# Kernel tuning notes

Measured on AMD Instinct MI355X. Metric: run time of the kernel, lower is better.

The kernel has to match this reference:

```python
import jax, jax.numpy as jnp
import numpy as np

B = 512
D = 512          # d_in == d_out for every layer
L = 3            # number of SprecherLayerBlocks
PHI_K = 100      # knots of monotonic phi spline
PHI_CAP_K = 100  # knots of Phi spline
PHI_IN = (-10.0, 10.0)
PHI_OUT = (-10.0, 10.0)


def setup_inputs() -> dict:
    key = jax.random.key(0)
    ks = jax.random.split(key, 8)
    x = jax.random.uniform(ks[0], (B, D), dtype=jnp.float32)
    # per-layer lambda vectors ~ N(0, 2/d_in)
    lambdas = jax.random.normal(ks[1], (L, D), dtype=jnp.float32) * np.sqrt(2.0 / D)
    eta = jnp.full((L,), 1.0 / (D + 10), dtype=jnp.float32)
    # monotonic phi: log_increments = log(1/K + 1e-6), identical per layer at init
    phi_log_inc = jnp.full((L, PHI_K), np.log(1.0 / PHI_K + 1e-6), dtype=jnp.float32)
    # Phi coeffs: linspace over codomain + small noise
    base = jnp.linspace(PHI_OUT[0], PHI_OUT[1], PHI_CAP_K, dtype=jnp.float32)
    Phi_coeffs = base[None, :] + jax.random.normal(ks[2], (L, PHI_CAP_K), dtype=jnp.float32) * 0.01
    # shared trainable range params (center/radius of domain & codomain)
    dc = jnp.float32((PHI_IN[0] + PHI_IN[1]) / 2.0)
    dr = jnp.float32((PHI_IN[1] - PHI_IN[0]) / 2.0)
    cc = jnp.float32((PHI_OUT[0] + PHI_OUT[1]) / 2.0)
    cr = jnp.float32((PHI_OUT[1] - PHI_OUT[0]) / 2.0)
    res_w = jnp.full((L,), 0.1, dtype=jnp.float32)
    output_scale = jnp.float32(1.0)
    return {"x": x, "lambdas": lambdas, "eta": eta, "phi_log_inc": phi_log_inc,
            "Phi_coeffs": Phi_coeffs, "dc": dc, "dr": dr, "cc": cc, "cr": cr,
            "res_w": res_w, "output_scale": output_scale}


def _interp(x, knots, coeffs, num_knots):
    # piecewise-linear eval: searchsorted + gather + lerp (x assumed pre-clamped)
    idx = jnp.clip(jnp.searchsorted(knots, x) - 1, 0, num_knots - 2)
    k0 = knots[idx]
    t = (x - k0) / (knots[idx + 1] - k0)
    return (1.0 - t) * coeffs[idx] + t * coeffs[idx + 1]


def reference(x, lambdas, eta, phi_log_inc, Phi_coeffs, dc, dr, cc, cr, res_w, output_scale):
    eps = 1e-8
    phi_knots = jnp.linspace(0.0, 1.0, PHI_K)
    norm_knots = jnp.linspace(0.0, 1.0, PHI_CAP_K)
    in_min, in_max = dc - dr, dc + dr
    out_min, out_max = cc - cr, cc + cr
    Phi_knots = norm_knots * (in_max - in_min) + in_min
    q = jnp.arange(D, dtype=x.dtype)  # q_values, Q_VALUES_FACTOR = 1
    h = x
    for l in range(L):
        # [B, d_in, d_out] shifted inputs, clamped to phi's (0,1) domain
        shifted = jnp.clip(h[:, :, None] + eta[l] * q[None, None, :], 0.0, 1.0)
        # monotonic phi coefficients in (0,1)
        inc = jax.nn.softplus(phi_log_inc[l])
        cum = jnp.cumsum(inc)
        phi_coef = cum / (cum[-1] + eps)
        phi_out = _interp(shifted, phi_knots, phi_coef, PHI_K)
        s = jnp.einsum('bio,i->bo', phi_out, lambdas[l]) + q
        # Phi spline with trainable range + renormalization by initial coeff min/max
        sc = jnp.clip(s, in_min, in_max)
        raw = _interp(sc, Phi_knots, Phi_coeffs[l], PHI_CAP_K)
        cmin = jax.lax.stop_gradient(Phi_coeffs[l].min())
        cmax = jax.lax.stop_gradient(Phi_coeffs[l].max())
        raw_n = jnp.clip((raw - cmin) / (cmax - cmin + eps), 0.0, 1.0)
        act = out_min + (out_max - out_min) * raw_n
        act = act + res_w[l] * h  # residual (d_in == d_out)
        if l == L - 1:
            act = act.sum(axis=1, keepdims=True)  # is_final block -> [B, 1]
        h = act
    return h * output_scale
```

## Files before the change

### kernel.cpp

```cpp
#include <hip/hip_runtime.h>

#define DD 512
#define LL 3
#define KK 100

#define WS_PHI     0
#define WS_CAP     600
#define WS_INMIN   1200
#define WS_INMAX   1201
#define WS_USCALE  1202
#define WS_OUTMIN  1203
#define WS_OUTSPAN 1204
#define WS_CMIN    1205
#define WS_INVDEN  1208
#define WS_OBEGIN  1211
#define WS_OEND    1214

__device__ __forceinline__ float fract_pos(float x) {
#if __has_builtin(__builtin_amdgcn_fractf)
  return __builtin_amdgcn_fractf(x);
#else
  return x - floorf(x);
#endif
}

__device__ __forceinline__ float med3f(float x, float lo, float hi) {
#if __has_builtin(__builtin_amdgcn_fmed3f)
  return __builtin_amdgcn_fmed3f(x, lo, hi);
#else
  return fminf(fmaxf(x, lo), hi);
#endif
}

__global__ __launch_bounds__(64) void prep_kernel(
    const float* __restrict__ lambdas,
    const float* __restrict__ phi_log_inc,
    const float* __restrict__ Phi_coeffs,
    const float* __restrict__ dc, const float* __restrict__ dr,
    const float* __restrict__ cc, const float* __restrict__ cr,
    float* __restrict__ ws)
{
  const int l = blockIdx.x;
  const int t = threadIdx.x;
  __shared__ float scum[104];

  const float in_min  = dc[0] - dr[0];
  const float in_max  = dc[0] + dr[0];
  const float out_min = cc[0] - cr[0];
  const float out_max = cc[0] + cr[0];
  if (l == 0 && t == 0) {
    ws[WS_INMIN]   = in_min;
    ws[WS_INMAX]   = in_max;
    ws[WS_USCALE]  = 99.0f / (in_max - in_min);
    ws[WS_OUTMIN]  = out_min;
    ws[WS_OUTSPAN] = out_max - out_min;
  }

  float a = log1pf(expf(phi_log_inc[l*KK + t]));
  #pragma unroll
  for (int d = 1; d < 64; d <<= 1) { float n = __shfl_up(a, d, 64); if (t >= d) a += n; }
  const float totA = __shfl(a, 63, 64);
  float b = (t < 36) ? log1pf(expf(phi_log_inc[l*KK + 64 + t])) : 0.0f;
  #pragma unroll
  for (int d = 1; d < 64; d <<= 1) { float n = __shfl_up(b, d, 64); if (t >= d) b += n; }
  b += totA;
  scum[t] = a;
  if (t < 36) scum[64 + t] = b;
  __syncthreads();
  const float inv = 1.0f / (scum[99] + 1e-8f);

  {
    float c0 = scum[t] * inv;
    float c1 = scum[t + 1] * inv;
    ws[WS_PHI + l*200 + 2*t]     = c0;
    ws[WS_PHI + l*200 + 2*t + 1] = c1 - c0;
    if (t < 36) {
      int j = 64 + t;
      float d0 = scum[j] * inv;
      float d1 = (j < 99) ? scum[j + 1] * inv - d0 : 0.0f;
      ws[WS_PHI + l*200 + 2*j]     = d0;
      ws[WS_PHI + l*200 + 2*j + 1] = d1;
    }
  }

  float C0  = Phi_coeffs[l*KK + t];
  float C64 = (t < 36) ? Phi_coeffs[l*KK + 64 + t] : C0;
  float cmn = fminf(C0, C64), cmx = fmaxf(C0, C64);
  #pragma unroll
  for (int d = 32; d; d >>= 1) {
    cmn = fminf(cmn, __shfl_xor(cmn, d, 64));
    cmx = fmaxf(cmx, __shfl_xor(cmx, d, 64));
  }
  {
    float n1 = Phi_coeffs[l*KK + t + 1];
    ws[WS_CAP + l*200 + 2*t]     = C0;
    ws[WS_CAP + l*200 + 2*t + 1] = n1 - C0;
    if (t < 36) {
      int j = 64 + t;
      float p0 = Phi_coeffs[l*KK + j];
      float p1 = (j < 99) ? Phi_coeffs[l*KK + j + 1] - p0 : 0.0f;
      ws[WS_CAP + l*200 + 2*j]     = p0;
      ws[WS_CAP + l*200 + 2*j + 1] = p1;
    }
  }

  float ns = 0.f, ps = 0.f;
  #pragma unroll
  for (int k = 0; k < 8; ++k) {
    float lv = lambdas[l*DD + t + 64*k];
    ns += fminf(lv, 0.f);
    ps += fmaxf(lv, 0.f);
  }
  #pragma unroll
  for (int d = 32; d; d >>= 1) {
    ns += __shfl_xor(ns, d, 64);
    ps += __shfl_xor(ps, d, 64);
  }
  if (t == 0) {
    ws[WS_CMIN + l]   = cmn;
    ws[WS_INVDEN + l] = 1.0f / (cmx - cmn + 1e-8f);
    float T_lo = in_min - ps;
    float T_hi = in_max - ns;
    int ob = (int)floorf(T_lo) + 1;
    if (ob < 0) ob = 0; if (ob > DD) ob = DD;
    int oe = (int)ceilf(T_hi);
    if (oe < ob) oe = ob; if (oe > DD) oe = DD;
    ((int*)ws)[WS_OBEGIN + l] = ob;
    ((int*)ws)[WS_OEND + l]   = oe;
  }
}

__device__ __forceinline__ float phistep(float h, float lam, float eo99,
                                         const float2* __restrict__ sphi, float acc)
{
  float xs = med3f(fmaf(h, 99.0f, eo99), 0.0f, 99.0f);
  int   j  = (int)xs;
  float t  = fract_pos(xs);
  float2 p = sphi[j];
  return fmaf(lam, fmaf(t, p.y, p.x), acc);
}

__global__ __launch_bounds__(512) void sprecher_kernel(
    const float* __restrict__ x,
    const float* __restrict__ lambdas,
    const float* __restrict__ eta,
    const float* __restrict__ res_w,
    const float* __restrict__ oscale,
    const float* __restrict__ ws,
    float* __restrict__ out)
{
  __shared__ __align__(16) float2 hl[DD];
  __shared__ float2 sphi[KK];
  __shared__ float2 scap[KK];
  __shared__ float  sarr[DD];
  __shared__ float  red[8];

  const int tid  = threadIdx.x;
  const int b    = blockIdx.x;
  const int lane = tid & 63;
  const int wave = tid >> 6;

  const float in_min   = ws[WS_INMIN];
  const float in_max   = ws[WS_INMAX];
  const float uscale   = ws[WS_USCALE];
  const float out_min  = ws[WS_OUTMIN];
  const float out_span = ws[WS_OUTSPAN];

  float hval = x[b*DD + tid];

  for (int l = 0; l < LL; ++l) {
    __syncthreads();
    hl[tid] = make_float2(hval, lambdas[l*DD + tid]);
    if (tid < KK)                          sphi[tid]       = ((const float2*)(ws + WS_PHI))[l*KK + tid];
    else if (tid >= 128 && tid < 128 + KK) scap[tid - 128] = ((const float2*)(ws + WS_CAP))[l*KK + (tid - 128)];
    __syncthreads();

    const float eta99  = 99.0f * eta[l];
    const float cmin   = ws[WS_CMIN + l];
    const float invden = ws[WS_INVDEN + l];
    const float rw     = res_w[l];
    const int   ob     = ((const int*)ws)[WS_OBEGIN + l];
    const int   oe     = ((const int*)ws)[WS_OEND + l];
    const int   nh     = oe - ob;

    const float4* hl4 = (const float4*)hl;
    for (int hidx = wave; hidx < nh; hidx += 8) {
      const int   o    = ob + hidx;
      const float eo99 = eta99 * (float)o;
      float acc0 = 0.f, acc1 = 0.f;
      const int base = lane * 4;
      #pragma unroll
      for (int uu = 0; uu < 4; ++uu) {
        float4 v = hl4[base + uu];
        acc0 = phistep(v.x, v.y, eo99, sphi, acc0);
        acc1 = phistep(v.z, v.w, eo99, sphi, acc1);
      }
      float acc = acc0 + acc1;
      #pragma unroll
      for (int d = 32; d; d >>= 1) acc += __shfl_xor(acc, d, 64);
      if (lane == 0) sarr[hidx] = acc;
    }
    __syncthreads();

    const int o = tid;
    float s;
    if (o < ob)       s = in_min;
    else if (o >= oe) s = in_max;
    else              s = sarr[o - ob] + (float)o;

    float sc  = fminf(fmaxf(s, in_min), in_max);
    float uq  = fminf((sc - in_min) * uscale, 99.0f);
    int   j   = (int)uq;
    float t2  = fract_pos(uq);
    float2 P  = scap[j];
    float raw = fmaf(t2, P.y, P.x);
    float rn  = med3f((raw - cmin) * invden, 0.0f, 1.0f);
    float act = fmaf(out_span, rn, out_min);
    hval = fmaf(rw, hval, act);
  }

  float v = hval;
  #pragma unroll
  for (int d = 32; d; d >>= 1) v += __shfl_xor(v, d, 64);
  if (lane == 0) red[wave] = v;
  __syncthreads();
  if (tid == 0) {
    float tot = 0.f;
    #pragma unroll
    for (int w = 0; w < 8; ++w) tot += red[w];
    out[b] = tot * oscale[0];
  }
}

extern "C" void kernel_launch(void* const* d_in, const int* in_sizes, int n_in,
                              void* d_out, int out_size, void* d_ws, size_t ws_size,
                              hipStream_t stream) {
  const float* x           = (const float*)d_in[0];
  const float* lambdas     = (const float*)d_in[1];
  const float* eta         = (const float*)d_in[2];
  const float* phi_log_inc = (const float*)d_in[3];
  const float* Phi_coeffs  = (const float*)d_in[4];
  const float* dc          = (const float*)d_in[5];
  const float* dr          = (const float*)d_in[6];
  const float* cc          = (const float*)d_in[7];
  const float* cr          = (const float*)d_in[8];
  const float* res_w       = (const float*)d_in[9];
  const float* oscale      = (const float*)d_in[10];
  float*       out         = (float*)d_out;
  float*       ws          = (float*)d_ws;

  prep_kernel<<<3, 64, 0, stream>>>(lambdas, phi_log_inc, Phi_coeffs, dc, dr, cc, cr, ws);
  sprecher_kernel<<<512, 512, 0, stream>>>(x, lambdas, eta, res_w, oscale, ws, out);
}
```

Measured before the change: 86.51 us.

## Fuse prep into main kernel and add uniform-knot linear fast path

Merges the small prep kernel into the main kernel: every block recomputes the spline tables, the Phi min/max and the active output range in shared memory, which removes one launch and the global workspace round trip. It adds a runtime check of whether the monotone phi coefficients are uniformly spaced. When they are, phi is evaluated as a straight line (xs*db+db) with no table gather. It also changes the hl float4 indexing so a wave's loads are consecutive. Each of the 512 blocks now repeats the prep work. The linear path depends on the uniform-increment input holding within a 3e-5 tolerance.

```diff
diff --git a/kernel.cpp b/kernel.cpp
--- a/kernel.cpp
+++ b/kernel.cpp
@@ -3,18 +3,6 @@
 #define DD 512
 #define LL 3
 #define KK 100
-
-#define WS_PHI     0
-#define WS_CAP     600
-#define WS_INMIN   1200
-#define WS_INMAX   1201
-#define WS_USCALE  1202
-#define WS_OUTMIN  1203
-#define WS_OUTSPAN 1204
-#define WS_CMIN    1205
-#define WS_INVDEN  1208
-#define WS_OBEGIN  1211
-#define WS_OEND    1214
 
 __device__ __forceinline__ float fract_pos(float x) {
 #if __has_builtin(__builtin_amdgcn_fractf)
@@ -32,191 +20,178 @@
 #endif
 }
 
-__global__ __launch_bounds__(64) void prep_kernel(
+__global__ __launch_bounds__(512) void sprecher_fused(
+    const float* __restrict__ x,
     const float* __restrict__ lambdas,
+    const float* __restrict__ eta,
     const float* __restrict__ phi_log_inc,
     const float* __restrict__ Phi_coeffs,
     const float* __restrict__ dc, const float* __restrict__ dr,
     const float* __restrict__ cc, const float* __restrict__ cr,
-    float* __restrict__ ws)
-{
-  const int l = blockIdx.x;
-  const int t = threadIdx.x;
-  __shared__ float scum[104];
-
-  const float in_min  = dc[0] - dr[0];
-  const float in_max  = dc[0] + dr[0];
-  const float out_min = cc[0] - cr[0];
-  const float out_max = cc[0] + cr[0];
-  if (l == 0 && t == 0) {
-    ws[WS_INMIN]   = in_min;
-    ws[WS_INMAX]   = in_max;
-    ws[WS_USCALE]  = 99.0f / (in_max - in_min);
-    ws[WS_OUTMIN]  = out_min;
-    ws[WS_OUTSPAN] = out_max - out_min;
-  }
-
-  float a = log1pf(expf(phi_log_inc[l*KK + t]));
-  #pragma unroll
-  for (int d = 1; d < 64; d <<= 1) { float n = __shfl_up(a, d, 64); if (t >= d) a += n; }
-  const float totA = __shfl(a, 63, 64);
-  float b = (t < 36) ? log1pf(expf(phi_log_inc[l*KK + 64 + t])) : 0.0f;
-  #pragma unroll
-  for (int d = 1; d < 64; d <<= 1) { float n = __shfl_up(b, d, 64); if (t >= d) b += n; }
-  b += totA;
-  scum[t] = a;
-  if (t < 36) scum[64 + t] = b;
-  __syncthreads();
-  const float inv = 1.0f / (scum[99] + 1e-8f);
-
-  {
-    float c0 = scum[t] * inv;
-    float c1 = scum[t + 1] * inv;
-    ws[WS_PHI + l*200 + 2*t]     = c0;
-    ws[WS_PHI + l*200 + 2*t + 1] = c1 - c0;
-    if (t < 36) {
-      int j = 64 + t;
-      float d0 = scum[j] * inv;
-      float d1 = (j < 99) ? scum[j + 1] * inv - d0 : 0.0f;
-      ws[WS_PHI + l*200 + 2*j]     = d0;
-      ws[WS_PHI + l*200 + 2*j + 1] = d1;
-    }
-  }
-
-  float C0  = Phi_coeffs[l*KK + t];
-  float C64 = (t < 36) ? Phi_coeffs[l*KK + 64 + t] : C0;
-  float cmn = fminf(C0, C64), cmx = fmaxf(C0, C64);
-  #pragma unroll
-  for (int d = 32; d; d >>= 1) {
-    cmn = fminf(cmn, __shfl_xor(cmn, d, 64));
-    cmx = fmaxf(cmx, __shfl_xor(cmx, d, 64));
-  }
-  {
-    float n1 = Phi_coeffs[l*KK + t + 1];
-    ws[WS_CAP + l*200 + 2*t]     = C0;
-    ws[WS_CAP + l*200 + 2*t + 1] = n1 - C0;
-    if (t < 36) {
-      int j = 64 + t;
-      float p0 = Phi_coeffs[l*KK + j];
-      float p1 = (j < 99) ? Phi_coeffs[l*KK + j + 1] - p0 : 0.0f;
-      ws[WS_CAP + l*200 + 2*j]     = p0;
-      ws[WS_CAP + l*200 + 2*j + 1] = p1;
-    }
-  }
-
-  float ns = 0.f, ps = 0.f;
-  #pragma unroll
-  for (int k = 0; k < 8; ++k) {
-    float lv = lambdas[l*DD + t + 64*k];
-    ns += fminf(lv, 0.f);
-    ps += fmaxf(lv, 0.f);
-  }
-  #pragma unroll
-  for (int d = 32; d; d >>= 1) {
-    ns += __shfl_xor(ns, d, 64);
-    ps += __shfl_xor(ps, d, 64);
-  }
-  if (t == 0) {
-    ws[WS_CMIN + l]   = cmn;
-    ws[WS_INVDEN + l] = 1.0f / (cmx - cmn + 1e-8f);
-    float T_lo = in_min - ps;
-    float T_hi = in_max - ns;
-    int ob = (int)floorf(T_lo) + 1;
-    if (ob < 0) ob = 0; if (ob > DD) ob = DD;
-    int oe = (int)ceilf(T_hi);
-    if (oe < ob) oe = ob; if (oe > DD) oe = DD;
-    ((int*)ws)[WS_OBEGIN + l] = ob;
-    ((int*)ws)[WS_OEND + l]   = oe;
-  }
-}
-
-__device__ __forceinline__ float phistep(float h, float lam, float eo99,
-                                         const float2* __restrict__ sphi, float acc)
-{
-  float xs = med3f(fmaf(h, 99.0f, eo99), 0.0f, 99.0f);
-  int   j  = (int)xs;
-  float t  = fract_pos(xs);
-  float2 p = sphi[j];
-  return fmaf(lam, fmaf(t, p.y, p.x), acc);
-}
-
-__global__ __launch_bounds__(512) void sprecher_kernel(
-    const float* __restrict__ x,
-    const float* __restrict__ lambdas,
-    const float* __restrict__ eta,
     const float* __restrict__ res_w,
     const float* __restrict__ oscale,
-    const float* __restrict__ ws,
     float* __restrict__ out)
 {
   __shared__ __align__(16) float2 hl[DD];
-  __shared__ float2 sphi[KK];
-  __shared__ float2 scap[KK];
+  __shared__ float2 sphi[LL][KK];
+  __shared__ float2 scap[LL][KK];
   __shared__ float  sarr[DD];
+  __shared__ float  wred[8][LL][2];
+  __shared__ float  scmin[LL], sinvden[LL];
+  __shared__ float2 slin[LL];
+  __shared__ int    sob[LL], soe[LL];
   __shared__ float  red[8];
 
   const int tid  = threadIdx.x;
-  const int b    = blockIdx.x;
   const int lane = tid & 63;
   const int wave = tid >> 6;
-
-  const float in_min   = ws[WS_INMIN];
-  const float in_max   = ws[WS_INMAX];
-  const float uscale   = ws[WS_USCALE];
-  const float out_min  = ws[WS_OUTMIN];
-  const float out_span = ws[WS_OUTSPAN];
-
+  const int b    = blockIdx.x;
+
+  const float in_min   = dc[0] - dr[0];
+  const float in_max   = dc[0] + dr[0];
+  const float out_min  = cc[0] - cr[0];
+  const float out_span = (cc[0] + cr[0]) - out_min;
+  const float uscale   = 99.0f / (in_max - in_min);
+
+  float lam[LL];
+  #pragma unroll
+  for (int l = 0; l < LL; ++l) lam[l] = lambdas[l*DD + tid];
   float hval = x[b*DD + tid];
+
+  #pragma unroll
+  for (int l = 0; l < LL; ++l) {
+    float ns = fminf(lam[l], 0.f), ps = fmaxf(lam[l], 0.f);
+    #pragma unroll
+    for (int d = 32; d; d >>= 1) { ns += __shfl_xor(ns, d, 64); ps += __shfl_xor(ps, d, 64); }
+    if (lane == 0) { wred[wave][l][0] = ns; wred[wave][l][1] = ps; }
+  }
+
+  if (wave < 3) {
+    const int l = wave;
+    auto sp = [](float v) { return fmaxf(v, 0.f) + log1pf(expf(-fabsf(v))); };
+    float a = sp(phi_log_inc[l*KK + lane]);
+    #pragma unroll
+    for (int d = 1; d < 64; d <<= 1) { float n = __shfl_up(a, d, 64); if (lane >= d) a += n; }
+    const float totA = __shfl(a, 63, 64);
+    float bb = (lane < 36) ? sp(phi_log_inc[l*KK + 64 + lane]) : 0.0f;
+    #pragma unroll
+    for (int d = 1; d < 64; d <<= 1) { float n = __shfl_up(bb, d, 64); if (lane >= d) bb += n; }
+    bb += totA;
+    const float T    = __shfl(bb, 35, 64);
+    const float inv  = 1.0f / (T + 1e-8f);
+    const float c64  = __shfl(bb, 0, 64);
+    const float a1   = __shfl_down(a, 1, 64);
+    const float cA   = a * inv;
+    const float nA   = ((lane == 63) ? c64 : a1) * inv;
+    sphi[l][lane] = make_float2(cA, nA - cA);
+    const float dbar = __shfl(a, 0, 64) * inv;
+    bool ok = (fabsf(cA - (float)(lane + 1) * dbar) <= 3e-5f) &&
+              (fabsf((nA - cA) - dbar) <= 3e-5f);
+    const float b1 = __shfl_down(bb, 1, 64);
+    if (lane < 36) {
+      const int j = 64 + lane;
+      const float cB = bb * inv;
+      const float nB = (j < 99) ? b1 * inv : cB;
+      sphi[l][j] = make_float2(cB, nB - cB);
+      bool okB = (fabsf(cB - (float)(j + 1) * dbar) <= 3e-5f) &&
+                 ((j == 99) || fabsf((nB - cB) - dbar) <= 3e-5f);
+      ok = ok && okB;
+    }
+    unsigned long long ball = __ballot(ok);
+    if (lane == 0) slin[l] = make_float2((ball == ~0ULL) ? 1.f : 0.f, dbar);
+  } else if (wave < 6) {
+    const int l = wave - 3;
+    const float C0  = Phi_coeffs[l*KK + lane];
+    const float C64 = (lane < 36) ? Phi_coeffs[l*KK + 64 + lane] : C0;
+    float cmn = fminf(C0, C64), cmx = fmaxf(C0, C64);
+    #pragma unroll
+    for (int d = 32; d; d >>= 1) {
+      cmn = fminf(cmn, __shfl_xor(cmn, d, 64));
+      cmx = fmaxf(cmx, __shfl_xor(cmx, d, 64));
+    }
+    const float n1 = Phi_coeffs[l*KK + lane + 1];
+    scap[l][lane] = make_float2(C0, n1 - C0);
+    if (lane < 36) {
+      const int j = 64 + lane;
+      const float p1 = (j < 99) ? Phi_coeffs[l*KK + j + 1] - C64 : 0.0f;
+      scap[l][j] = make_float2(C64, p1);
+    }
+    if (lane == 0) { scmin[l] = cmn; sinvden[l] = 1.0f / (cmx - cmn + 1e-8f); }
+  }
+  __syncthreads();
+
+  if (tid < LL) {
+    float ns = 0.f, ps = 0.f;
+    for (int w = 0; w < 8; ++w) { ns += wred[w][tid][0]; ps += wred[w][tid][1]; }
+    int ob = (int)floorf(in_min - ps) + 1; ob = max(0, min(DD, ob));
+    int oe = (int)ceilf(in_max - ns);      oe = max(ob, min(DD, oe));
+    sob[tid] = ob; soe[tid] = oe;
+  }
+
+  float eta99v[LL], rwv[LL];
+  #pragma unroll
+  for (int l = 0; l < LL; ++l) { eta99v[l] = 99.0f * eta[l]; rwv[l] = res_w[l]; }
 
   for (int l = 0; l < LL; ++l) {
     __syncthreads();
-    hl[tid] = make_float2(hval, lambdas[l*DD + tid]);
-    if (tid < KK)                          sphi[tid]       = ((const float2*)(ws + WS_PHI))[l*KK + tid];
-    else if (tid >= 128 && tid < 128 + KK) scap[tid - 128] = ((const float2*)(ws + WS_CAP))[l*KK + (tid - 128)];
+    hl[tid] = make_float2(hval, lam[l]);
     __syncthreads();
-
-    const float eta99  = 99.0f * eta[l];
-    const float cmin   = ws[WS_CMIN + l];
-    const float invden = ws[WS_INVDEN + l];
-    const float rw     = res_w[l];
-    const int   ob     = ((const int*)ws)[WS_OBEGIN + l];
-    const int   oe     = ((const int*)ws)[WS_OEND + l];
-    const int   nh     = oe - ob;
-
+    const int   ob = sob[l], oe = soe[l], nh = oe - ob;
+    const float e99 = eta99v[l];
+    const float2 li = slin[l];
     const float4* hl4 = (const float4*)hl;
-    for (int hidx = wave; hidx < nh; hidx += 8) {
-      const int   o    = ob + hidx;
-      const float eo99 = eta99 * (float)o;
-      float acc0 = 0.f, acc1 = 0.f;
-      const int base = lane * 4;
-      #pragma unroll
-      for (int uu = 0; uu < 4; ++uu) {
-        float4 v = hl4[base + uu];
-        acc0 = phistep(v.x, v.y, eo99, sphi, acc0);
-        acc1 = phistep(v.z, v.w, eo99, sphi, acc1);
+
+    if (li.x > 0.5f) {
+      const float db = li.y;
+      for (int hidx = wave; hidx < nh; hidx += 8) {
+        const float eo99 = e99 * (float)(ob + hidx);
+        float acc0 = 0.f, acc1 = 0.f;
+        #pragma unroll
+        for (int uu = 0; uu < 4; ++uu) {
+          float4 v = hl4[uu*64 + lane];
+          float xs0 = med3f(fmaf(v.x, 99.0f, eo99), 0.0f, 99.0f);
+          float xs1 = med3f(fmaf(v.z, 99.0f, eo99), 0.0f, 99.0f);
+          acc0 = fmaf(v.y, fmaf(xs0, db, db), acc0);
+          acc1 = fmaf(v.w, fmaf(xs1, db, db), acc1);
+        }
+        float acc = acc0 + acc1;
+        #pragma unroll
+        for (int d = 32; d; d >>= 1) acc += __shfl_xor(acc, d, 64);
+        if (lane == 0) sarr[hidx] = acc;
       }
-      float acc = acc0 + acc1;
-      #pragma unroll
-      for (int d = 32; d; d >>= 1) acc += __shfl_xor(acc, d, 64);
-      if (lane == 0) sarr[hidx] = acc;
+    } else {
+      const float2* tp = sphi[l];
+      for (int hidx = wave; hidx < nh; hidx += 8) {
+        const float eo99 = e99 * (float)(ob + hidx);
+        float acc0 = 0.f, acc1 = 0.f;
+        #pragma unroll
+        for (int uu = 0; uu < 4; ++uu) {
+          float4 v = hl4[uu*64 + lane];
+          { float xs = med3f(fmaf(v.x, 99.0f, eo99), 0.0f, 99.0f);
+            int j = (int)xs; float t = fract_pos(xs); float2 p = tp[j];
+            acc0 = fmaf(v.y, fmaf(t, p.y, p.x), acc0); }
+          { float xs = med3f(fmaf(v.z, 99.0f, eo99), 0.0f, 99.0f);
+            int j = (int)xs; float t = fract_pos(xs); float2 p = tp[j];
+            acc1 = fmaf(v.w, fmaf(t, p.y, p.x), acc1); }
+        }
+        float acc = acc0 + acc1;
+        #pragma unroll
+        for (int d = 32; d; d >>= 1) acc += __shfl_xor(acc, d, 64);
+        if (lane == 0) sarr[hidx] = acc;
+      }
     }
     __syncthreads();
 
     const int o = tid;
-    float s;
-    if (o < ob)       s = in_min;
-    else if (o >= oe) s = in_max;
-    else              s = sarr[o - ob] + (float)o;
-
+    float s = (o < ob) ? in_min : (o >= oe) ? in_max : sarr[o - ob] + (float)o;
     float sc  = fminf(fmaxf(s, in_min), in_max);
     float uq  = fminf((sc - in_min) * uscale, 99.0f);
     int   j   = (int)uq;
     float t2  = fract_pos(uq);
-    float2 P  = scap[j];
+    float2 P  = scap[l][j];
     float raw = fmaf(t2, P.y, P.x);
-    float rn  = med3f((raw - cmin) * invden, 0.0f, 1.0f);
-    float act = fmaf(out_span, rn, out_min);
-    hval = fmaf(rw, hval, act);
+    float rn  = med3f((raw - scmin[l]) * sinvden[l], 0.0f, 1.0f);
+    hval = fmaf(rwv[l], hval, fmaf(out_span, rn, out_min));
   }
 
   float v = hval;
@@ -226,7 +201,6 @@
   __syncthreads();
   if (tid == 0) {
     float tot = 0.f;
-    #pragma unroll
     for (int w = 0; w < 8; ++w) tot += red[w];
     out[b] = tot * oscale[0];
   }
@@ -247,8 +221,7 @@
   const float* res_w       = (const float*)d_in[9];
   const float* oscale      = (const float*)d_in[10];
   float*       out         = (float*)d_out;
-  float*       ws          = (float*)d_ws;
-
-  prep_kernel<<<3, 64, 0, stream>>>(lambdas, phi_log_inc, Phi_coeffs, dc, dr, cc, cr, ws);
-  sprecher_kernel<<<512, 512, 0, stream>>>(x, lambdas, eta, res_w, oscale, ws, out);
-}
+
+  sprecher_fused<<<512, 512, 0, stream>>>(x, lambdas, eta, phi_log_inc, Phi_coeffs,
+                                          dc, dr, cc, cr, res_w, oscale, out);
+}
```

Measured after the change: 81.64 us. 5.6% less time.
